# Optimization experiments

Hardware: AMD Instinct MI355X
Metric: run time of the kernel (lower is better)

## Reference

```python
import jax, jax.numpy as jnp
import numpy as np


def _rconv(x, w, b):
    # reflection-pad 1 then 3x3 valid conv (same spatial size), NCHW/OIHW
    xp = jnp.pad(x, ((0, 0), (0, 0), (1, 1), (1, 1)), mode='reflect')
    y = jax.lax.conv_general_dilated(
        xp, w, window_strides=(1, 1), padding='VALID',
        dimension_numbers=('NCHW', 'OIHW', 'NCHW'))
    return y + b[None, :, None, None]


def setup_inputs() -> dict:
    key = jax.random.key(0)
    ks = jax.random.split(key, 12)
    B, C, H, W = 4, 256, 64, 64
    IC = 128  # inter_channels
    s = lambda fan_in: 1.0 / np.sqrt(fan_in)
    return {
        'query_feat': jax.random.normal(ks[0], (B, C, H, W), jnp.float32),
        'key_feat': jax.random.normal(ks[1], (B, C, H, W), jnp.float32),
        # 1x1 conv projections (stored as [out, in])
        'w_theta': jax.random.normal(ks[2], (IC, C), jnp.float32) * s(C),
        'b_theta': jnp.zeros((IC,), jnp.float32),
        'w_phi': jax.random.normal(ks[3], (IC, C), jnp.float32) * s(C),
        'b_phi': jnp.zeros((IC,), jnp.float32),
        # post-correlation block: conv(1->32), residual(32), conv(32->1)
        'w_in': jax.random.normal(ks[4], (32, 1, 3, 3), jnp.float32) * s(9),
        'b_in': jnp.zeros((32,), jnp.float32),
        'w_r1': jax.random.normal(ks[5], (32, 32, 3, 3), jnp.float32) * s(32 * 9),
        'b_r1': jnp.zeros((32,), jnp.float32),
        'w_r2': jax.random.normal(ks[6], (32, 32, 3, 3), jnp.float32) * s(32 * 9),
        'b_r2': jnp.zeros((32,), jnp.float32),
        'w_out': jax.random.normal(ks[7], (1, 32, 3, 3), jnp.float32) * s(32 * 9),
        'b_out': jnp.zeros((1,), jnp.float32),
    }


def reference(query_feat, key_feat, w_theta, b_theta, w_phi, b_phi,
              w_in, b_in, w_r1, b_r1, w_r2, b_r2, w_out, b_out):
    B, C, H, W = query_feat.shape
    N = H * W
    # 1x1 conv projections, flattened to sequences
    theta = jnp.einsum('oc,bchw->bohw', w_theta, query_feat) + b_theta[None, :, None, None]
    phi = jnp.einsum('oc,bchw->bohw', w_phi, key_feat) + b_phi[None, :, None, None]
    theta = theta.reshape(B, -1, N).transpose(0, 2, 1)  # [B, N, IC]
    phi = phi.reshape(B, -1, N)                          # [B, IC, N]
    # correlation matrix [B, N, N] then max over key positions
    f = jnp.matmul(theta, phi)
    sim = jnp.max(f, axis=-1).reshape(B, 1, H, W)
    # post-correlation conv refinement
    h = _rconv(sim, w_in, b_in)                      # 1 -> 32
    r = jax.nn.relu(_rconv(h, w_r1, b_r1))           # residual block
    r = _rconv(r, w_r2, b_r2)
    h = h + r
    out = _rconv(h, w_out, b_out)                    # 32 -> 1
    return out
```

## Files before the change

### kernel.cpp

```cpp
#include <hip/hip_runtime.h>

#define B_ 4
#define C_ 256
#define HH 64
#define WW 64
#define N_ 4096
#define IC_ 128
#define JC_ 8

typedef __attribute__((ext_vector_type(8))) short bf16x8;
typedef __attribute__((ext_vector_type(4))) float f32x4;

__device__ __forceinline__ short f2bf(float f) {
    unsigned u = __builtin_bit_cast(unsigned, f);
    unsigned r = (u + 0x7FFFu + ((u >> 16) & 1u)) >> 16;
    return (short)r;
}

__device__ __forceinline__ int refl(int v) {
    return v < 0 ? -v : (v > 63 ? 126 - v : v);
}

__global__ __launch_bounds__(256) void k_cvt_w(const float* __restrict__ wt,
                                               const float* __restrict__ wp,
                                               short* __restrict__ wtb,
                                               short* __restrict__ wpb) {
    int i = blockIdx.x * 256 + threadIdx.x;
    wtb[i] = f2bf(wt[i]);
    wpb[i] = f2bf(wp[i]);
}

__global__ __launch_bounds__(256) void k_project(
    const float* __restrict__ qf, const float* __restrict__ kf,
    const short* __restrict__ wq, const short* __restrict__ wk,
    const float* __restrict__ bq, const float* __restrict__ bk,
    short* __restrict__ outq, short* __restrict__ outk) {
    int z = blockIdx.z;
    const float* x = z ? kf : qf;
    const short* wbf = z ? wk : wq;
    const float* bias = z ? bk : bq;
    short* outT = z ? outk : outq;

    int b = blockIdx.y;
    int n0 = blockIdx.x * 64;
    int t = threadIdx.x;
    int lane = t & 63, wv = t >> 6;
    int l15 = lane & 15, q4 = lane >> 4;
    const float* xb = x + (size_t)b * C_ * N_;

    __shared__ float xs[2][32][65];

    f32x4 acc[8];
#pragma unroll
    for (int cf = 0; cf < 8; cf++) acc[cf] = (f32x4){0.f, 0.f, 0.f, 0.f};

    {
        int i0 = t, i1 = t + 256;
        int r0 = i0 >> 4, c0 = i0 & 15;
        int r1 = i1 >> 4, c1 = i1 & 15;
        f32x4 v0 = *(const f32x4*)(xb + (size_t)r0 * N_ + n0 + c0 * 4);
        f32x4 v1 = *(const f32x4*)(xb + (size_t)r1 * N_ + n0 + c1 * 4);
#pragma unroll
        for (int s = 0; s < 4; s++) xs[0][r0][c0 * 4 + s] = v0[s];
#pragma unroll
        for (int s = 0; s < 4; s++) xs[0][r1][c1 * 4 + s] = v1[s];
    }

    for (int ks = 0; ks < 8; ks++) {
        __syncthreads();
        int buf = ks & 1;
        if (ks < 7) {
            int cb = (ks + 1) * 32;
            int i0 = t, i1 = t + 256;
            int r0 = i0 >> 4, c0 = i0 & 15;
            int r1 = i1 >> 4, c1 = i1 & 15;
            f32x4 v0 = *(const f32x4*)(xb + (size_t)(cb + r0) * N_ + n0 + c0 * 4);
            f32x4 v1 = *(const f32x4*)(xb + (size_t)(cb + r1) * N_ + n0 + c1 * 4);
#pragma unroll
            for (int s = 0; s < 4; s++) xs[buf ^ 1][r0][c0 * 4 + s] = v0[s];
#pragma unroll
            for (int s = 0; s < 4; s++) xs[buf ^ 1][r1][c1 * 4 + s] = v1[s];
        }
        int cbase = ks * 32 + q4 * 8;
        bf16x8 a;
#pragma unroll
        for (int j = 0; j < 8; j++) a[j] = f2bf(xs[buf][q4 * 8 + j][wv * 16 + l15]);
#pragma unroll
        for (int cf = 0; cf < 8; cf++) {
            const short* wp = wbf + (cf * 16 + l15) * C_ + cbase;
            bf16x8 bfr = *(const bf16x8*)wp;
            acc[cf] = __builtin_amdgcn_mfma_f32_16x16x32_bf16(a, bfr, acc[cf], 0, 0, 0);
        }
    }
#pragma unroll
    for (int cf = 0; cf < 8; cf++) {
        int ic = cf * 16 + l15;
        float bv = bias[ic];
#pragma unroll
        for (int r = 0; r < 4; r++) {
            int n = n0 + wv * 16 + q4 * 4 + r;
            outT[((size_t)b * N_ + n) * IC_ + ic] = f2bf(acc[cf][r] + bv);
        }
    }
}

__global__ __launch_bounds__(256) void k_corr(const short* __restrict__ thetaT,
                                              const short* __restrict__ phiT,
                                              float* __restrict__ simp) {
    __shared__ short ph[64][136];
    __shared__ float red[4][64];

    int b = blockIdx.z;
    int jc = blockIdx.y;
    int i0 = blockIdx.x * 64;
    int t = threadIdx.x;
    int lane = t & 63, wv = t >> 6;
    int l15 = lane & 15, q4 = lane >> 4;

    const short* thb = thetaT + ((size_t)b * N_ + i0) * IC_;
    const short* phb = phiT + ((size_t)b * N_ + jc * (N_ / JC_)) * IC_;

    bf16x8 afr[4][4];
#pragma unroll
    for (int rf = 0; rf < 4; rf++)
#pragma unroll
        for (int ks = 0; ks < 4; ks++)
            afr[rf][ks] = *(const bf16x8*)(thb + (size_t)(rf * 16 + l15) * IC_ + ks * 32 + q4 * 8);

    f32x4 rmax[4];
#pragma unroll
    for (int rf = 0; rf < 4; rf++) rmax[rf] = (f32x4){-3.0e38f, -3.0e38f, -3.0e38f, -3.0e38f};

    for (int j0 = 0; j0 < N_ / JC_; j0 += 64) {
#pragma unroll
        for (int k = 0; k < 4; k++) {
            int id = t + k * 256;
            int row = id >> 4, c8 = id & 15;
            *(bf16x8*)(&ph[row][c8 * 8]) =
                *(const bf16x8*)(phb + (size_t)(j0 + row) * IC_ + c8 * 8);
        }
        __syncthreads();

        bf16x8 bfr[4];
#pragma unroll
        for (int ks = 0; ks < 4; ks++)
            bfr[ks] = *(const bf16x8*)(&ph[wv * 16 + l15][ks * 32 + q4 * 8]);

#pragma unroll
        for (int rf = 0; rf < 4; rf++) {
            f32x4 a2 = (f32x4){0.f, 0.f, 0.f, 0.f};
#pragma unroll
            for (int ks = 0; ks < 4; ks++)
                a2 = __builtin_amdgcn_mfma_f32_16x16x32_bf16(afr[rf][ks], bfr[ks], a2, 0, 0, 0);
#pragma unroll
            for (int r = 0; r < 4; r++) rmax[rf][r] = fmaxf(rmax[rf][r], a2[r]);
        }
        __syncthreads();
    }

#pragma unroll
    for (int rf = 0; rf < 4; rf++) {
#pragma unroll
        for (int r = 0; r < 4; r++) {
            float v = rmax[rf][r];
            v = fmaxf(v, __shfl_xor(v, 1));
            v = fmaxf(v, __shfl_xor(v, 2));
            v = fmaxf(v, __shfl_xor(v, 4));
            v = fmaxf(v, __shfl_xor(v, 8));
            if (l15 == 0) red[wv][rf * 16 + q4 * 4 + r] = v;
        }
    }
    __syncthreads();
    if (t < 64) {
        float m = fmaxf(fmaxf(red[0][t], red[1][t]), fmaxf(red[2][t], red[3][t]));
        simp[((size_t)(b * JC_ + jc)) * N_ + i0 + t] = m;
    }
}

__global__ __launch_bounds__(256) void k_conv_in(const float* __restrict__ simp,
                                                 const float* __restrict__ w,
                                                 const float* __restrict__ bias,
                                                 float* __restrict__ h) {
    int y = blockIdx.x, b = blockIdx.y;
    int t = threadIdx.x;
    int oc = t >> 3, x8 = t & 7;
    __shared__ float srow[3][66];
    const float* sb = simp + (size_t)b * JC_ * N_;
    if (t < 192) {
        int r = t >> 6, x = t & 63;
        int idx = refl(y - 1 + r) * 64 + x;
        float v = -3.0e38f;
#pragma unroll
        for (int jc = 0; jc < JC_; jc++) v = fmaxf(v, sb[jc * N_ + idx]);
        srow[r][x + 1] = v;
    }
    if (t < 3) {
        int gy = refl(y - 1 + t);
        float vl = -3.0e38f, vr = -3.0e38f;
#pragma unroll
        for (int jc = 0; jc < JC_; jc++) {
            vl = fmaxf(vl, sb[jc * N_ + gy * 64 + 1]);
            vr = fmaxf(vr, sb[jc * N_ + gy * 64 + 62]);
        }
        srow[t][0] = vl;
        srow[t][65] = vr;
    }
    __syncthreads();

    float wr[9];
#pragma unroll
    for (int k = 0; k < 9; k++) wr[k] = w[oc * 9 + k];
    float bv = bias[oc];
    float acc[8];
#pragma unroll
    for (int xi = 0; xi < 8; xi++) acc[xi] = bv;
#pragma unroll
    for (int ky = 0; ky < 3; ky++)
#pragma unroll
        for (int kx = 0; kx < 3; kx++) {
            float wv2 = wr[ky * 3 + kx];
#pragma unroll
            for (int xi = 0; xi < 8; xi++) acc[xi] += wv2 * srow[ky][x8 * 8 + xi + kx];
        }
    float* op = h + (((size_t)b * 32 + oc) * 64 + y) * 64 + x8 * 8;
#pragma unroll
    for (int xi = 0; xi < 8; xi++) op[xi] = acc[xi];
}

template <bool RELU, bool ADD>
__global__ __launch_bounds__(256) void k_conv_r(const float* __restrict__ in,
                                                const float* __restrict__ w,
                                                const float* __restrict__ bias,
                                                float* __restrict__ out,
                                                const float* __restrict__ add) {
    int y = blockIdx.x, b = blockIdx.z;
    int oc0 = blockIdx.y * 16;
    int t = threadIdx.x;
    __shared__ float tile[32][3][68];

#pragma unroll
    for (int r = 0; r < 3; r++) {
        int gy = refl(y - 1 + r);
#pragma unroll
        for (int i = 0; i < 2; i++) {
            int idx = t + i * 256;
            int ic = idx >> 4, c4 = idx & 15;
            f32x4 v = *(const f32x4*)(in + (((size_t)b * 32 + ic) * 64 + gy) * 64 + c4 * 4);
#pragma unroll
            for (int s = 0; s < 4; s++) tile[ic][r][c4 * 4 + s + 1] = v[s];
        }
    }
    if (t < 96) {
        int ic = t / 3, r = t - ic * 3;
        int gy = refl(y - 1 + r);
        const float* row = in + (((size_t)b * 32 + ic) * 64 + gy) * 64;
        tile[ic][r][0] = row[1];
        tile[ic][r][65] = row[62];
    }
    __syncthreads();

    int oc = oc0 + (t >> 4), x4 = (t & 15) * 4;
    float bv = bias[oc];
    float acc[4];
#pragma unroll
    for (int xi = 0; xi < 4; xi++) acc[xi] = bv;

    for (int ic = 0; ic < 32; ic++) {
        const float* wp = w + ((size_t)oc * 32 + ic) * 9;
        float w0 = wp[0], w1 = wp[1], w2 = wp[2], w3 = wp[3], w4 = wp[4];
        float w5 = wp[5], w6 = wp[6], w7 = wp[7], w8 = wp[8];
        float xr[3][8];
#pragma unroll
        for (int r = 0; r < 3; r++) {
            const float* rowp = &tile[ic][r][x4];
            f32x4 A = *(const f32x4*)(rowp);
            f32x4 Bv = *(const f32x4*)(rowp + 4);
            xr[r][0] = A[0]; xr[r][1] = A[1]; xr[r][2] = A[2]; xr[r][3] = A[3];
            xr[r][4] = Bv[0]; xr[r][5] = Bv[1]; xr[r][6] = Bv[2]; xr[r][7] = Bv[3];
        }
#pragma unroll
        for (int xi = 0; xi < 4; xi++) {
            acc[xi] += w0 * xr[0][xi] + w1 * xr[0][xi + 1] + w2 * xr[0][xi + 2] +
                       w3 * xr[1][xi] + w4 * xr[1][xi + 1] + w5 * xr[1][xi + 2] +
                       w6 * xr[2][xi] + w7 * xr[2][xi + 1] + w8 * xr[2][xi + 2];
        }
    }
    size_t off = (((size_t)b * 32 + oc) * 64 + y) * 64 + x4;
#pragma unroll
    for (int xi = 0; xi < 4; xi++) {
        float v = acc[xi];
        if (RELU) v = fmaxf(v, 0.f);
        if (ADD) v += add[off + xi];
        out[off + xi] = v;
    }
}

__global__ __launch_bounds__(256) void k_conv_out(const float* __restrict__ hb,
                                                  const float* __restrict__ w,
                                                  const float* __restrict__ bias,
                                                  float* __restrict__ outp) {
    int y = blockIdx.x, b = blockIdx.y;
    int t = threadIdx.x;
    int x = t & 63, g = t >> 6;
    __shared__ float red[4][64];
    float acc = 0.f;
#pragma unroll
    for (int i = 0; i < 8; i++) {
        int ic = g * 8 + i;
        const float* wp = w + ic * 9;
#pragma unroll
        for (int ky = 0; ky < 3; ky++) {
            int gy = refl(y + ky - 1);
            const float* row = hb + (((size_t)b * 32 + ic) * 64 + gy) * 64;
#pragma unroll
            for (int kx = 0; kx < 3; kx++) {
                int gx = refl(x + kx - 1);
                acc += wp[ky * 3 + kx] * row[gx];
            }
        }
    }
    red[g][x] = acc;
    __syncthreads();
    if (t < 64) {
        outp[((size_t)b * 64 + y) * 64 + x] =
            bias[0] + red[0][t] + red[1][t] + red[2][t] + red[3][t];
    }
}

extern "C" void kernel_launch(void* const* d_in, const int* in_sizes, int n_in,
                              void* d_out, int out_size, void* d_ws, size_t ws_size,
                              hipStream_t stream) {
    const float* q = (const float*)d_in[0];
    const float* kf = (const float*)d_in[1];
    const float* w_theta = (const float*)d_in[2];
    const float* b_theta = (const float*)d_in[3];
    const float* w_phi = (const float*)d_in[4];
    const float* b_phi = (const float*)d_in[5];
    const float* w_in = (const float*)d_in[6];
    const float* b_in = (const float*)d_in[7];
    const float* w_r1 = (const float*)d_in[8];
    const float* b_r1 = (const float*)d_in[9];
    const float* w_r2 = (const float*)d_in[10];
    const float* b_r2 = (const float*)d_in[11];
    const float* w_out = (const float*)d_in[12];
    const float* b_out = (const float*)d_in[13];
    float* out = (float*)d_out;

    char* ws = (char*)d_ws;
    short* thetaT = (short*)(ws);
    short* phiT = (short*)(ws + 4194304);
    short* wthb = (short*)(ws + 8388608);
    short* wphb = (short*)(ws + 8454144);
    float* simp = (float*)(ws + 8519680);
    float* h = (float*)(ws);
    float* r = (float*)(ws + 2097152);

    k_cvt_w<<<128, 256, 0, stream>>>(w_theta, w_phi, wthb, wphb);
    k_project<<<dim3(64, 4, 2), 256, 0, stream>>>(q, kf, wthb, wphb, b_theta, b_phi,
                                                  thetaT, phiT);
    k_corr<<<dim3(64, JC_, 4), 256, 0, stream>>>(thetaT, phiT, simp);
    k_conv_in<<<dim3(64, 4), 256, 0, stream>>>(simp, w_in, b_in, h);
    k_conv_r<true, false><<<dim3(64, 2, 4), 256, 0, stream>>>(h, w_r1, b_r1, r, nullptr);
    k_conv_r<false, true><<<dim3(64, 2, 4), 256, 0, stream>>>(r, w_r2, b_r2, h, h);
    k_conv_out<<<dim3(64, 4), 256, 0, stream>>>(h, w_out, b_out, out);
}
```

Before: 191.7 us.

## Retile correlation kernel: per-wave query rows, shared phi tile, double-buffered loads

Each block now covers 256 query rows: every wave keeps its own 64 theta rows in registers, and all four waves compute against the whole 64-column phi tile in LDS. Before, the four waves split the phi columns and the block covered only 64 rows. Each phi tile loaded into shared memory is therefore reused by four times as many rows, so phi traffic per output drops and the grid shrinks to a quarter of the blocks. The phi loads are double-buffered so the next tile is fetched while the current one is consumed, with one barrier per iteration. The cross-wave LDS reduction is gone, since each wave writes its own row maxima, but there are far fewer blocks (512) to fill the GPU.

```diff
diff --git a/kernel.cpp b/kernel.cpp
--- a/kernel.cpp
+++ b/kernel.cpp
@@ -107,17 +107,15 @@
 __global__ __launch_bounds__(256) void k_corr(const short* __restrict__ thetaT,
                                               const short* __restrict__ phiT,
                                               float* __restrict__ simp) {
-    __shared__ short ph[64][136];
-    __shared__ float red[4][64];
-
-    int b = blockIdx.z;
-    int jc = blockIdx.y;
-    int i0 = blockIdx.x * 64;
-    int t = threadIdx.x;
-    int lane = t & 63, wv = t >> 6;
+    __shared__ short ph[2][64][136];
+
+    int b = blockIdx.z, jc = blockIdx.y;
+    int i0 = blockIdx.x * 256;
+    int t = threadIdx.x;
+    int lane = t & 63, w = t >> 6;
     int l15 = lane & 15, q4 = lane >> 4;
 
-    const short* thb = thetaT + ((size_t)b * N_ + i0) * IC_;
+    const short* thb = thetaT + ((size_t)b * N_ + i0 + w * 64) * IC_;
     const short* phb = phiT + ((size_t)b * N_ + jc * (N_ / JC_)) * IC_;
 
     bf16x8 afr[4][4];
@@ -127,39 +125,47 @@
         for (int ks = 0; ks < 4; ks++)
             afr[rf][ks] = *(const bf16x8*)(thb + (size_t)(rf * 16 + l15) * IC_ + ks * 32 + q4 * 8);
 
+    int srow = t >> 4, sc8 = t & 15;
+#pragma unroll
+    for (int k = 0; k < 4; k++)
+        *(bf16x8*)(&ph[0][srow + k * 16][sc8 * 8]) =
+            *(const bf16x8*)(phb + (size_t)(srow + k * 16) * IC_ + sc8 * 8);
+
     f32x4 rmax[4];
 #pragma unroll
     for (int rf = 0; rf < 4; rf++) rmax[rf] = (f32x4){-3.0e38f, -3.0e38f, -3.0e38f, -3.0e38f};
 
-    for (int j0 = 0; j0 < N_ / JC_; j0 += 64) {
-#pragma unroll
-        for (int k = 0; k < 4; k++) {
-            int id = t + k * 256;
-            int row = id >> 4, c8 = id & 15;
-            *(bf16x8*)(&ph[row][c8 * 8]) =
-                *(const bf16x8*)(phb + (size_t)(j0 + row) * IC_ + c8 * 8);
-        }
+    for (int it = 0; it < 8; it++) {
+        int buf = it & 1;
         __syncthreads();
-
-        bf16x8 bfr[4];
-#pragma unroll
-        for (int ks = 0; ks < 4; ks++)
-            bfr[ks] = *(const bf16x8*)(&ph[wv * 16 + l15][ks * 32 + q4 * 8]);
-
-#pragma unroll
-        for (int rf = 0; rf < 4; rf++) {
-            f32x4 a2 = (f32x4){0.f, 0.f, 0.f, 0.f};
+        if (it < 7) {
+            int j0 = (it + 1) * 64;
+#pragma unroll
+            for (int k = 0; k < 4; k++)
+                *(bf16x8*)(&ph[buf ^ 1][srow + k * 16][sc8 * 8]) =
+                    *(const bf16x8*)(phb + (size_t)(j0 + srow + k * 16) * IC_ + sc8 * 8);
+        }
+#pragma unroll
+        for (int jf = 0; jf < 4; jf++) {
+            bf16x8 bfr[4];
 #pragma unroll
             for (int ks = 0; ks < 4; ks++)
-                a2 = __builtin_amdgcn_mfma_f32_16x16x32_bf16(afr[rf][ks], bfr[ks], a2, 0, 0, 0);
-#pragma unroll
-            for (int r = 0; r < 4; r++) rmax[rf][r] = fmaxf(rmax[rf][r], a2[r]);
-        }
-        __syncthreads();
-    }
-
-#pragma unroll
-    for (int rf = 0; rf < 4; rf++) {
+                bfr[ks] = *(const bf16x8*)(&ph[buf][jf * 16 + l15][ks * 32 + q4 * 8]);
+#pragma unroll
+            for (int rf = 0; rf < 4; rf++) {
+                f32x4 a2 = (f32x4){0.f, 0.f, 0.f, 0.f};
+#pragma unroll
+                for (int ks = 0; ks < 4; ks++)
+                    a2 = __builtin_amdgcn_mfma_f32_16x16x32_bf16(afr[rf][ks], bfr[ks], a2, 0, 0, 0);
+#pragma unroll
+                for (int r = 0; r < 4; r++) rmax[rf][r] = fmaxf(rmax[rf][r], a2[r]);
+            }
+        }
+    }
+
+    float red[4][4];
+#pragma unroll
+    for (int rf = 0; rf < 4; rf++)
 #pragma unroll
         for (int r = 0; r < 4; r++) {
             float v = rmax[rf][r];
@@ -167,13 +173,14 @@
             v = fmaxf(v, __shfl_xor(v, 2));
             v = fmaxf(v, __shfl_xor(v, 4));
             v = fmaxf(v, __shfl_xor(v, 8));
-            if (l15 == 0) red[wv][rf * 16 + q4 * 4 + r] = v;
-        }
-    }
-    __syncthreads();
-    if (t < 64) {
-        float m = fmaxf(fmaxf(red[0][t], red[1][t]), fmaxf(red[2][t], red[3][t]));
-        simp[((size_t)(b * JC_ + jc)) * N_ + i0 + t] = m;
+            red[rf][r] = v;
+        }
+    if (l15 == 0) {
+        float* sp = simp + ((size_t)(b * JC_ + jc)) * N_ + i0 + w * 64;
+#pragma unroll
+        for (int rf = 0; rf < 4; rf++)
+#pragma unroll
+            for (int r = 0; r < 4; r++) sp[rf * 16 + q4 * 4 + r] = red[rf][r];
     }
 }
 
@@ -358,7 +365,7 @@
     k_cvt_w<<<128, 256, 0, stream>>>(w_theta, w_phi, wthb, wphb);
     k_project<<<dim3(64, 4, 2), 256, 0, stream>>>(q, kf, wthb, wphb, b_theta, b_phi,
                                                   thetaT, phiT);
-    k_corr<<<dim3(64, JC_, 4), 256, 0, stream>>>(thetaT, phiT, simp);
+    k_corr<<<dim3(16, JC_, 4), 256, 0, stream>>>(thetaT, phiT, simp);
     k_conv_in<<<dim3(64, 4), 256, 0, stream>>>(simp, w_in, b_in, h);
     k_conv_r<true, false><<<dim3(64, 2, 4), 256, 0, stream>>>(h, w_r1, b_r1, r, nullptr);
     k_conv_r<false, true><<<dim3(64, 2, 4), 256, 0, stream>>>(r, w_r2, b_r2, h, h);
```

Result: faster. 167.9 us (-12.4%).
